# Kernel tuning notes

Measured on AMD Instinct MI355X. Metric: run time of the kernel, lower is better.

## Reference

```python
import jax, jax.numpy as jnp
import numpy as np

B, T, D = 4, 2048, 1024
H = 16
HD = D // H  # 64


def setup_inputs() -> dict:
    key = jax.random.key(0)
    ks = jax.random.split(key, 9)
    x = jax.random.normal(ks[0], (B, T, D), dtype=jnp.float32)
    s = 0.02
    Wq = jax.random.normal(ks[1], (D, D), dtype=jnp.float32) * s
    bq = jnp.zeros((D,), dtype=jnp.float32)
    Wk = jax.random.normal(ks[2], (D, D), dtype=jnp.float32) * s
    bk = jnp.zeros((D,), dtype=jnp.float32)
    Wv = jax.random.normal(ks[3], (D, D), dtype=jnp.float32) * s
    bv = jnp.zeros((D,), dtype=jnp.float32)
    Wo = jax.random.normal(ks[4], (D, D), dtype=jnp.float32) * s
    bo = jnp.zeros((D,), dtype=jnp.float32)
    return {"x": x, "Wq": Wq, "bq": bq, "Wk": Wk, "bk": bk,
            "Wv": Wv, "bv": bv, "Wo": Wo, "bo": bo}


def reference(x, Wq, bq, Wk, bk, Wv, bv, Wo, bo):
    Bn, Tn, Dn = x.shape
    # projections -> [B, H, T, HD]
    def split_heads(y):
        return y.reshape(Bn, Tn, H, HD).transpose(0, 2, 1, 3)
    Q = split_heads(x @ Wq + bq)
    K = split_heads(x @ Wk + bk)
    V = split_heads(x @ Wv + bv)
    scores = jnp.einsum('bhqd,bhkd->bhqk', Q, K) / jnp.sqrt(jnp.float32(HD))
    attn = jax.nn.softmax(scores, axis=-1)           # [B, H, T, T]
    attn_weights = attn.mean(axis=1)                 # [B, T, T] (head-averaged)
    out = jnp.einsum('bhqk,bhkd->bhqd', attn, V)     # [B, H, T, HD]
    out = out.transpose(0, 2, 1, 3).reshape(Bn, Tn, Dn)
    out = out @ Wo + bo                              # [B, T, D]
    # pooling weight: mean over query dim -> [B, 1, T] -> transpose -> [B, T, 1]
    pool_w = attn_weights.mean(axis=1, keepdims=True).transpose(0, 2, 1)
    pooled = (out * pool_w).sum(axis=1)              # [B, D]
    return pooled
```

## Files before the change

### kernel.cpp

```cpp
#include <hip/hip_runtime.h>
#include <hip/hip_bf16.h>
#include <stdint.h>

#define B_ 4
#define T_ 2048
#define D_ 1024
#define H_ 16
#define HD_ 64

#define QSCALE 0.1803368801111244f

typedef __bf16 bf16_t;
typedef __bf16 bf16x8 __attribute__((ext_vector_type(8)));
typedef __bf16 bf16x4 __attribute__((ext_vector_type(4)));
typedef float f32x4 __attribute__((ext_vector_type(4)));

__device__ __forceinline__ f32x4 mfma16(bf16x8 a, bf16x8 b, f32x4 c) {
  return __builtin_amdgcn_mfma_f32_16x16x32_bf16(a, b, c, 0, 0, 0);
}

__device__ __forceinline__ void gload_lds16(const bf16_t* g, bf16_t* l) {
  __builtin_amdgcn_global_load_lds(
      (const __attribute__((address_space(1))) unsigned int*)g,
      (__attribute__((address_space(3))) unsigned int*)l, 16, 0, 0);
}

__device__ __forceinline__ float exp2g(float x) {
  return __builtin_amdgcn_exp2f(x);
}

__global__ __launch_bounds__(256) void conv_x(const float* __restrict__ x,
                                              bf16_t* __restrict__ xb) {
  size_t i = ((size_t)blockIdx.x * 256 + threadIdx.x) * 8;
  float4 a = *(const float4*)(x + i);
  float4 b = *(const float4*)(x + i + 4);
  bf16x8 v;
  v[0] = (bf16_t)a.x; v[1] = (bf16_t)a.y; v[2] = (bf16_t)a.z; v[3] = (bf16_t)a.w;
  v[4] = (bf16_t)b.x; v[5] = (bf16_t)b.y; v[6] = (bf16_t)b.z; v[7] = (bf16_t)b.w;
  *(bf16x8*)(xb + i) = v;
}

__global__ __launch_bounds__(256) void conv_wt3(
    const float* __restrict__ Wq, const float* __restrict__ Wk,
    const float* __restrict__ Wv, bf16_t* __restrict__ WtAll) {
  __shared__ float Ls[64][65];
  const int tid = threadIdx.x;
  const int z = blockIdx.z;
  const float* W = (z == 0) ? Wq : (z == 1) ? Wk : Wv;
  bf16_t* Wt = WtAll + (size_t)z * 1024 * D_;
  const int k0 = blockIdx.y * 64, n0 = blockIdx.x * 64;
  const int rr = tid >> 4, cc = (tid & 15) * 4;
#pragma unroll
  for (int it = 0; it < 4; ++it) {
    int r = rr + it * 16;
    float4 v = *(const float4*)(W + (size_t)(k0 + r) * D_ + n0 + cc);
    Ls[r][cc] = v.x; Ls[r][cc + 1] = v.y; Ls[r][cc + 2] = v.z; Ls[r][cc + 3] = v.w;
  }
  __syncthreads();
#pragma unroll
  for (int it = 0; it < 4; ++it) {
    int nl = rr + it * 16;
    bf16x4 o;
    o[0] = (bf16_t)Ls[cc][nl];     o[1] = (bf16_t)Ls[cc + 1][nl];
    o[2] = (bf16_t)Ls[cc + 2][nl]; o[3] = (bf16_t)Ls[cc + 3][nl];
    *(bf16x4*)(Wt + (size_t)(n0 + nl) * D_ + k0 + cc) = o;
  }
}

__global__ __launch_bounds__(256) void gemm_qkv(
    const bf16_t* __restrict__ A, const bf16_t* __restrict__ Bt,
    const float* __restrict__ bq, const float* __restrict__ bk,
    const float* __restrict__ bv,
    bf16_t* __restrict__ Qo, bf16_t* __restrict__ Ko, bf16_t* __restrict__ Vo)
{
  __shared__ __align__(16) bf16_t As[128 * 64];
  __shared__ __align__(16) bf16_t Bs[128 * 64];
  const int tid = threadIdx.x, lane = tid & 63, wv = tid >> 6;
  const int wr = wv >> 1, wc = wv & 1;
  const int wg = blockIdx.x;
  const int xcd = wg & 7;
  const int local = wg >> 3;
  const int mb = xcd * 8 + (local & 7);
  const int nb = local >> 3;
  const int m0 = mb * 128, n0 = nb * 128;
  const int mode = nb >> 3;
  const int lr = lane & 15, lg = lane >> 4;
  const int srow = wv * 8 + (lane >> 3);
  const int scol = (lane & 7) * 8;

  f32x4 acc[4][4] = {};

  for (int k0 = 0; k0 < D_; k0 += 64) {
    __syncthreads();
#pragma unroll
    for (int i = 0; i < 4; ++i) {
      gload_lds16(A + (size_t)(m0 + i * 32 + srow) * D_ + k0 + scol,
                  &As[(i * 32 + wv * 8) * 64]);
      gload_lds16(Bt + (size_t)(n0 + i * 32 + srow) * D_ + k0 + scol,
                  &Bs[(i * 32 + wv * 8) * 64]);
    }
    __syncthreads();

#pragma unroll
    for (int ks = 0; ks < 2; ++ks) {
      bf16x8 af[4], bfr[4];
#pragma unroll
      for (int i = 0; i < 4; ++i)
        af[i] = *(const bf16x8*)&As[(wr * 64 + i * 16 + lr) * 64 + ks * 32 + lg * 8];
#pragma unroll
      for (int j = 0; j < 4; ++j)
        bfr[j] = *(const bf16x8*)&Bs[(wc * 64 + j * 16 + lr) * 64 + ks * 32 + lg * 8];
#pragma unroll
      for (int i = 0; i < 4; ++i)
#pragma unroll
        for (int j = 0; j < 4; ++j)
          acc[i][j] = mfma16(af[i], bfr[j], acc[i][j]);
    }
  }

  bf16_t* out = (mode == 0) ? Qo : (mode == 1) ? Ko : Vo;
  const float* bias = (mode == 0) ? bq : (mode == 1) ? bk : bv;
  const float scale = (mode == 0) ? QSCALE : 1.0f;
  const int nl0 = n0 - mode * 1024;
#pragma unroll
  for (int j = 0; j < 4; ++j) {
    int n = nl0 + wc * 64 + j * 16 + lr;
    float bval = bias[n];
    int h = n >> 6, d = n & 63;
#pragma unroll
    for (int i = 0; i < 4; ++i)
#pragma unroll
      for (int r = 0; r < 4; ++r) {
        int m = m0 + wr * 64 + i * 16 + lg * 4 + r;
        int b = m >> 11, t = m & (T_ - 1);
        float val = (acc[i][j][r] + bval) * scale;
        out[(((size_t)(b * H_ + h)) * T_ + t) * HD_ + d] = (bf16_t)val;
      }
  }
}

__global__ __launch_bounds__(256) void qkv_gemm_f32(
    const float* __restrict__ x, const float* __restrict__ W,
    const float* __restrict__ bias, bf16_t* __restrict__ out, float scale)
{
  __shared__ bf16_t As[128][40];
  __shared__ bf16_t Bs[128][40];
  const int tid = threadIdx.x, lane = tid & 63, wv = tid >> 6;
  const int wr = wv >> 1, wc = wv & 1;
  const int m0 = blockIdx.y * 128, n0 = blockIdx.x * 128;
  const int lr = lane & 15, lg = lane >> 4;
  f32x4 acc[4][4] = {};
  const int xr = tid >> 3, xc = tid & 7;
  const int wk = tid >> 5, wn = tid & 31;

  for (int k0 = 0; k0 < D_; k0 += 32) {
    __syncthreads();
#pragma unroll
    for (int it = 0; it < 4; ++it) {
      int r = xr + it * 32;
      float4 v = *(const float4*)(x + (size_t)(m0 + r) * D_ + k0 + xc * 4);
      bf16_t* dst = &As[r][xc * 4];
      dst[0] = (bf16_t)v.x; dst[1] = (bf16_t)v.y;
      dst[2] = (bf16_t)v.z; dst[3] = (bf16_t)v.w;
    }
#pragma unroll
    for (int it = 0; it < 4; ++it) {
      int k = wk + it * 8;
      float4 v = *(const float4*)(W + (size_t)(k0 + k) * D_ + n0 + wn * 4);
      Bs[wn * 4 + 0][k] = (bf16_t)v.x;
      Bs[wn * 4 + 1][k] = (bf16_t)v.y;
      Bs[wn * 4 + 2][k] = (bf16_t)v.z;
      Bs[wn * 4 + 3][k] = (bf16_t)v.w;
    }
    __syncthreads();
    bf16x8 af[4], bfr[4];
#pragma unroll
    for (int i = 0; i < 4; ++i) af[i]  = *(const bf16x8*)&As[wr * 64 + i * 16 + lr][lg * 8];
#pragma unroll
    for (int j = 0; j < 4; ++j) bfr[j] = *(const bf16x8*)&Bs[wc * 64 + j * 16 + lr][lg * 8];
#pragma unroll
    for (int i = 0; i < 4; ++i)
#pragma unroll
      for (int j = 0; j < 4; ++j)
        acc[i][j] = mfma16(af[i], bfr[j], acc[i][j]);
  }

#pragma unroll
  for (int j = 0; j < 4; ++j) {
    int n = n0 + wc * 64 + j * 16 + lr;
    float bval = bias[n];
    int h = n >> 6, d = n & 63;
#pragma unroll
    for (int i = 0; i < 4; ++i)
#pragma unroll
      for (int r = 0; r < 4; ++r) {
        int m = m0 + wr * 64 + i * 16 + lg * 4 + r;
        int b = m >> 11, t = m & (T_ - 1);
        float val = (acc[i][j][r] + bval) * scale;
        out[(((size_t)(b * H_ + h)) * T_ + t) * HD_ + d] = (bf16_t)val;
      }
  }
}

__global__ __launch_bounds__(256) void attn_rowsum(
    const bf16_t* __restrict__ Q, const bf16_t* __restrict__ K,
    float* __restrict__ Lsum)
{
  const int tid = threadIdx.x, lane = tid & 63, wv = tid >> 6;
  const int lr = lane & 15, lg = lane >> 4;
  const int wg = blockIdx.x;
  const int p_ = wg >> 3;
  const int bh = (wg & 7) * 8 + (p_ >> 4);
  const int rem = p_ & 15;
  const int qc = rem >> 1;
  const int th = rem & 1;
  const int q0w = qc * 256 + wv * 64;

  const bf16_t* Qb = Q + (size_t)bh * T_ * HD_;
  const bf16_t* Kb = K + (size_t)bh * T_ * HD_;

  bf16x8 qa[4][2];
#pragma unroll
  for (int qq = 0; qq < 4; ++qq)
#pragma unroll
    for (int ks = 0; ks < 2; ++ks)
      qa[qq][ks] = *(const bf16x8*)(Qb + (size_t)(q0w + qq * 16 + lr) * HD_ +
                                    ks * 32 + lg * 8);

  float acc[4][4] = {};

  const int tlo = th * (T_ / 2), thi = tlo + T_ / 2;
  for (int tb = tlo; tb < thi; tb += 64) {
#pragma unroll
    for (int ts = 0; ts < 2; ++ts) {
      const int tA = tb + ts * 32 + lr;
      const int tB = tA + 16;
      bf16x8 kA0 = *(const bf16x8*)(Kb + (size_t)tA * HD_ + lg * 8);
      bf16x8 kA1 = *(const bf16x8*)(Kb + (size_t)tA * HD_ + 32 + lg * 8);
      bf16x8 kB0 = *(const bf16x8*)(Kb + (size_t)tB * HD_ + lg * 8);
      bf16x8 kB1 = *(const bf16x8*)(Kb + (size_t)tB * HD_ + 32 + lg * 8);
#pragma unroll
      for (int qq = 0; qq < 4; ++qq) {
        f32x4 sA = {}, sB = {};
        __builtin_amdgcn_s_setprio(1);
        sA = mfma16(qa[qq][0], kA0, sA);
        sA = mfma16(qa[qq][1], kA1, sA);
        sB = mfma16(qa[qq][0], kB0, sB);
        sB = mfma16(qa[qq][1], kB1, sB);
        __builtin_amdgcn_s_setprio(0);
#pragma unroll
        for (int r = 0; r < 4; ++r)
          acc[qq][r] += exp2g(sA[r]) + exp2g(sB[r]);
      }
    }
  }

#pragma unroll
  for (int qq = 0; qq < 4; ++qq)
#pragma unroll
    for (int r = 0; r < 4; ++r) {
      float v = acc[qq][r];
      v += __shfl_xor(v, 1); v += __shfl_xor(v, 2);
      v += __shfl_xor(v, 4); v += __shfl_xor(v, 8);
      acc[qq][r] = v;
    }
  if (lr == 0) {
#pragma unroll
    for (int qq = 0; qq < 4; ++qq)
#pragma unroll
      for (int r = 0; r < 4; ++r)
        atomicAdd(&Lsum[(size_t)bh * T_ + q0w + qq * 16 + lg * 4 + r],
                  acc[qq][r]);
  }
}

__global__ __launch_bounds__(256) void inv_l(float* __restrict__ L) {
  size_t i = ((size_t)blockIdx.x * 256 + threadIdx.x) * 4;
  float4 v = *(float4*)(L + i);
  v.x = 1.f / v.x; v.y = 1.f / v.y; v.z = 1.f / v.z; v.w = 1.f / v.w;
  *(float4*)(L + i) = v;
}

__global__ __launch_bounds__(256) void attn_colsum(
    const bf16_t* __restrict__ Q, const bf16_t* __restrict__ K,
    const float* __restrict__ Linv, float* __restrict__ colsum)
{
  const int tid = threadIdx.x, lane = tid & 63, wv = tid >> 6;
  const int lr = lane & 15, lg = lane >> 4;
  const int wg = blockIdx.x;
  const int p_ = wg >> 3;
  const int bh = (wg & 7) * 8 + (p_ >> 4);
  const int rem = p_ & 15;
  const int tc = rem >> 2;
  const int qs = rem & 3;
  const int b = bh >> 4;
  const int t0w = tc * 512 + wv * 128;

  const bf16_t* Qb = Q + (size_t)bh * T_ * HD_;
  const bf16_t* Kb = K + (size_t)bh * T_ * HD_;
  const float* Lb = Linv + (size_t)bh * T_;

  bf16x8 kf[8][2];
#pragma unroll
  for (int tt = 0; tt < 8; ++tt)
#pragma unroll
    for (int ks = 0; ks < 2; ++ks)
      kf[tt][ks] = *(const bf16x8*)(Kb + (size_t)(t0w + tt * 16 + lr) * HD_ +
                                    ks * 32 + lg * 8);

  float acc[8][4] = {};

  const int qlo = qs * (T_ / 4), qhi = qlo + T_ / 4;
  for (int qb = qlo; qb < qhi; qb += 64) {
#pragma unroll
    for (int qp = 0; qp < 2; ++qp) {
      const int qA = qb + qp * 32 + lr;
      const int qB = qA + 16;
      bf16x8 qA0 = *(const bf16x8*)(Qb + (size_t)qA * HD_ + lg * 8);
      bf16x8 qA1 = *(const bf16x8*)(Qb + (size_t)qA * HD_ + 32 + lg * 8);
      bf16x8 qB0 = *(const bf16x8*)(Qb + (size_t)qB * HD_ + lg * 8);
      bf16x8 qB1 = *(const bf16x8*)(Qb + (size_t)qB * HD_ + 32 + lg * 8);
      const float lvA = Lb[qA];
      const float lvB = Lb[qB];
#pragma unroll
      for (int tt = 0; tt < 8; ++tt) {
        f32x4 sA = {}, sB = {};
        __builtin_amdgcn_s_setprio(1);
        sA = mfma16(kf[tt][0], qA0, sA);
        sA = mfma16(kf[tt][1], qA1, sA);
        sB = mfma16(kf[tt][0], qB0, sB);
        sB = mfma16(kf[tt][1], qB1, sB);
        __builtin_amdgcn_s_setprio(0);
#pragma unroll
        for (int r = 0; r < 4; ++r) {
          acc[tt][r] = fmaf(exp2g(sA[r]), lvA, acc[tt][r]);
          acc[tt][r] = fmaf(exp2g(sB[r]), lvB, acc[tt][r]);
        }
      }
    }
  }

#pragma unroll
  for (int tt = 0; tt < 8; ++tt)
#pragma unroll
    for (int r = 0; r < 4; ++r) {
      float v = acc[tt][r];
      v += __shfl_xor(v, 1); v += __shfl_xor(v, 2);
      v += __shfl_xor(v, 4); v += __shfl_xor(v, 8);
      acc[tt][r] = v;
    }
  if (lr == 0) {
#pragma unroll
    for (int tt = 0; tt < 8; ++tt)
#pragma unroll
      for (int r = 0; r < 4; ++r)
        atomicAdd(&colsum[b * T_ + t0w + tt * 16 + lg * 4 + r], acc[tt][r]);
  }
}

__global__ __launch_bounds__(256) void attn_w2(
    const bf16_t* __restrict__ Q, const bf16_t* __restrict__ K,
    const float* __restrict__ Linv, const float* __restrict__ CS,
    float* __restrict__ w2)
{
  const int tid = threadIdx.x, lane = tid & 63, wv = tid >> 6;
  const int lr = lane & 15, lg = lane >> 4;
  const int wg = blockIdx.x;
  const int p_ = wg >> 3;
  const int bh = (wg & 7) * 8 + (p_ >> 4);
  const int rem = p_ & 15;
  const int tc = rem >> 2;
  const int qs = rem & 3;
  const int b = bh >> 4;
  const int t0w = tc * 512 + wv * 128;

  const bf16_t* Qb = Q + (size_t)bh * T_ * HD_;
  const bf16_t* Kb = K + (size_t)bh * T_ * HD_;
  const float* Lb = Linv + (size_t)bh * T_;
  const float* Cb = CS + (size_t)b * T_;

  bf16x8 kf[8][2];
#pragma unroll
  for (int tt = 0; tt < 8; ++tt)
#pragma unroll
    for (int ks = 0; ks < 2; ++ks)
      kf[tt][ks] = *(const bf16x8*)(Kb + (size_t)(t0w + tt * 16 + lr) * HD_ +
                                    ks * 32 + lg * 8);

  float acc[8][4] = {};

  const int qlo = qs * (T_ / 4), qhi = qlo + T_ / 4;
  for (int qb = qlo; qb < qhi; qb += 64) {
#pragma unroll
    for (int qp = 0; qp < 2; ++qp) {
      const int qA = qb + qp * 32 + lr;
      const int qB = qA + 16;
      bf16x8 qA0 = *(const bf16x8*)(Qb + (size_t)qA * HD_ + lg * 8);
      bf16x8 qA1 = *(const bf16x8*)(Qb + (size_t)qA * HD_ + 32 + lg * 8);
      bf16x8 qB0 = *(const bf16x8*)(Qb + (size_t)qB * HD_ + lg * 8);
      bf16x8 qB1 = *(const bf16x8*)(Qb + (size_t)qB * HD_ + 32 + lg * 8);
      const float lvA = Cb[qA] * Lb[qA] * (1.f / 32768.f);
      const float lvB = Cb[qB] * Lb[qB] * (1.f / 32768.f);
#pragma unroll
      for (int tt = 0; tt < 8; ++tt) {
        f32x4 sA = {}, sB = {};
        __builtin_amdgcn_s_setprio(1);
        sA = mfma16(kf[tt][0], qA0, sA);
        sA = mfma16(kf[tt][1], qA1, sA);
        sB = mfma16(kf[tt][0], qB0, sB);
        sB = mfma16(kf[tt][1], qB1, sB);
        __builtin_amdgcn_s_setprio(0);
#pragma unroll
        for (int r = 0; r < 4; ++r) {
          acc[tt][r] = fmaf(exp2g(sA[r]), lvA, acc[tt][r]);
          acc[tt][r] = fmaf(exp2g(sB[r]), lvB, acc[tt][r]);
        }
      }
    }
  }

#pragma unroll
  for (int tt = 0; tt < 8; ++tt)
#pragma unroll
    for (int r = 0; r < 4; ++r) {
      float v = acc[tt][r];
      v += __shfl_xor(v, 1); v += __shfl_xor(v, 2);
      v += __shfl_xor(v, 4); v += __shfl_xor(v, 8);
      acc[tt][r] = v;
    }
  if (lr == 0) {
#pragma unroll
    for (int tt = 0; tt < 8; ++tt)
#pragma unroll
      for (int r = 0; r < 4; ++r)
        atomicAdd(&w2[(size_t)bh * T_ + t0w + tt * 16 + lg * 4 + r],
                  acc[tt][r]);
  }
}

__global__ __launch_bounds__(256) void pool_wv(
    const bf16_t* __restrict__ V, const float* __restrict__ W2,
    float* __restrict__ pre)
{
  __shared__ float sm[256];
  const int wg = blockIdx.x;
  const int bh = wg >> 3, sc = wg & 7;
  const int b = bh >> 4, h = bh & 15;
  const int tid = threadIdx.x, d = tid & 63, tg = tid >> 6;
  const bf16_t* Vb = V + (size_t)bh * T_ * HD_ + (size_t)sc * 256 * HD_;
  const float* wb = W2 + (size_t)bh * T_ + sc * 256;
  float acc = 0.f;
  for (int s = tg; s < 256; s += 4)
    acc += wb[s] * (float)Vb[(size_t)s * HD_ + d];
  sm[tid] = acc;
  __syncthreads();
  if (tid < 64) {
    float s = sm[tid] + sm[tid + 64] + sm[tid + 128] + sm[tid + 192];
    atomicAdd(&pre[b * D_ + h * 64 + tid], s);
  }
}

__global__ __launch_bounds__(256) void out_acc(
    const float* __restrict__ pre, const float* __restrict__ Wo,
    const float* __restrict__ bo, float* __restrict__ out)
{
  const int dc = blockIdx.x & 3, kb = blockIdx.x >> 2;
  const int d = dc * 256 + threadIdx.x;
  const int k0 = kb * 32;
  float acc0 = 0.f, acc1 = 0.f, acc2 = 0.f, acc3 = 0.f;
#pragma unroll
  for (int kk = 0; kk < 32; ++kk) {
    const int k = k0 + kk;
    const float w = Wo[(size_t)k * D_ + d];
    acc0 = fmaf(pre[k],            w, acc0);
    acc1 = fmaf(pre[D_ + k],       w, acc1);
    acc2 = fmaf(pre[2 * D_ + k],   w, acc2);
    acc3 = fmaf(pre[3 * D_ + k],   w, acc3);
  }
  if (kb == 0) {
    const float bd = bo[d];
    acc0 += bd; acc1 += bd; acc2 += bd; acc3 += bd;
  }
  atomicAdd(&out[d],           acc0);
  atomicAdd(&out[D_ + d],      acc1);
  atomicAdd(&out[2 * D_ + d],  acc2);
  atomicAdd(&out[3 * D_ + d],  acc3);
}

extern "C" void kernel_launch(void* const* d_in, const int* in_sizes, int n_in,
                              void* d_out, int out_size, void* d_ws, size_t ws_size,
                              hipStream_t stream)
{
  (void)in_sizes; (void)n_in; (void)out_size;
  const float* x  = (const float*)d_in[0];
  const float* Wq = (const float*)d_in[1];
  const float* bq = (const float*)d_in[2];
  const float* Wk = (const float*)d_in[3];
  const float* bk = (const float*)d_in[4];
  const float* Wv = (const float*)d_in[5];
  const float* bv = (const float*)d_in[6];
  const float* Wo = (const float*)d_in[7];
  const float* bo = (const float*)d_in[8];
  float* out = (float*)d_out;

  char* ws = (char*)d_ws;
  const size_t MB = 1ull << 20;
  const size_t KB = 1024;
  bf16_t* Qw = (bf16_t*)(ws);
  bf16_t* Kw = (bf16_t*)(ws + 16 * MB);
  bf16_t* Vw = (bf16_t*)(ws + 32 * MB);
  bf16_t* XB = (bf16_t*)(ws + 48 * MB);
  const size_t need_fast = 72 * MB;
  const bool fast = ws_size >= need_fast;

  size_t soff = fast ? 70 * MB : 64 * MB;
  float* LV  = (float*)(ws + soff);
  float* CS  = (float*)(ws + soff + 512 * KB);
  float* PRE = (float*)(ws + soff + 544 * KB);
  float* W2  = (float*)(ws + soff + 560 * KB);
  dim3 blk(256, 1, 1);

  if (fast) {
    bf16_t* WtAll = (bf16_t*)(ws + 64 * MB);
    conv_x<<<dim3((B_ * T_ * D_) / (256 * 8), 1, 1), blk, 0, stream>>>(x, XB);
    conv_wt3<<<dim3(16, 16, 3), blk, 0, stream>>>(Wq, Wk, Wv, WtAll);
    gemm_qkv<<<dim3(1536, 1, 1), blk, 0, stream>>>(XB, WtAll, bq, bk, bv,
                                                   Qw, Kw, Vw);
  } else {
    qkv_gemm_f32<<<dim3(8, 64, 1), blk, 0, stream>>>(x, Wq, bq, Qw, QSCALE);
    qkv_gemm_f32<<<dim3(8, 64, 1), blk, 0, stream>>>(x, Wk, bk, Kw, 1.0f);
    qkv_gemm_f32<<<dim3(8, 64, 1), blk, 0, stream>>>(x, Wv, bv, Vw, 1.0f);
  }

  hipMemsetAsync(LV, 0, 1072 * KB, stream);
  hipMemsetAsync(out, 0, (size_t)B_ * D_ * sizeof(float), stream);

  attn_rowsum<<<dim3(1024, 1, 1), blk, 0, stream>>>(Qw, Kw, LV);
  inv_l<<<dim3((B_ * H_ * T_) / (256 * 4), 1, 1), blk, 0, stream>>>(LV);
  attn_colsum<<<dim3(1024, 1, 1), blk, 0, stream>>>(Qw, Kw, LV, CS);
  attn_w2<<<dim3(1024, 1, 1), blk, 0, stream>>>(Qw, Kw, LV, CS, W2);
  pool_wv<<<dim3(512, 1, 1), blk, 0, stream>>>(Vw, W2, PRE);
  out_acc<<<dim3(128, 1, 1), blk, 0, stream>>>(PRE, Wo, bo, out);
}
```

Before: 301.1 us.

## Enlarge QKV GEMM tile to 256x128 with 512 threads and fold reciprocal into consumers

```diff
diff --git a/kernel.cpp b/kernel.cpp
--- a/kernel.cpp
+++ b/kernel.cpp
@@ -27,6 +27,10 @@
 
 __device__ __forceinline__ float exp2g(float x) {
   return __builtin_amdgcn_exp2f(x);
+}
+
+__device__ __forceinline__ float rcpg(float x) {
+  return __builtin_amdgcn_rcpf(x);
 }
 
 __global__ __launch_bounds__(256) void conv_x(const float* __restrict__ x,
@@ -67,38 +71,39 @@
   }
 }
 
-__global__ __launch_bounds__(256) void gemm_qkv(
+__global__ __launch_bounds__(512) void gemm_qkv(
     const bf16_t* __restrict__ A, const bf16_t* __restrict__ Bt,
     const float* __restrict__ bq, const float* __restrict__ bk,
     const float* __restrict__ bv,
     bf16_t* __restrict__ Qo, bf16_t* __restrict__ Ko, bf16_t* __restrict__ Vo)
 {
-  __shared__ __align__(16) bf16_t As[128 * 64];
+  __shared__ __align__(16) bf16_t As[256 * 64];
   __shared__ __align__(16) bf16_t Bs[128 * 64];
   const int tid = threadIdx.x, lane = tid & 63, wv = tid >> 6;
   const int wr = wv >> 1, wc = wv & 1;
   const int wg = blockIdx.x;
   const int xcd = wg & 7;
   const int local = wg >> 3;
-  const int mb = xcd * 8 + (local & 7);
-  const int nb = local >> 3;
-  const int m0 = mb * 128, n0 = nb * 128;
+  const int mb = xcd * 4 + (local & 3);
+  const int nb = local >> 2;
+  const int m0 = mb * 256, n0 = nb * 128;
   const int mode = nb >> 3;
   const int lr = lane & 15, lg = lane >> 4;
-  const int srow = wv * 8 + (lane >> 3);
-  const int scol = (lane & 7) * 8;
+  const int srow = tid >> 3;
+  const int scol = (tid & 7) * 8;
 
   f32x4 acc[4][4] = {};
 
   for (int k0 = 0; k0 < D_; k0 += 64) {
     __syncthreads();
 #pragma unroll
-    for (int i = 0; i < 4; ++i) {
-      gload_lds16(A + (size_t)(m0 + i * 32 + srow) * D_ + k0 + scol,
-                  &As[(i * 32 + wv * 8) * 64]);
-      gload_lds16(Bt + (size_t)(n0 + i * 32 + srow) * D_ + k0 + scol,
-                  &Bs[(i * 32 + wv * 8) * 64]);
-    }
+    for (int i = 0; i < 4; ++i)
+      gload_lds16(A + (size_t)(m0 + i * 64 + srow) * D_ + k0 + scol,
+                  &As[(i * 64 + (wv << 3)) * 64]);
+#pragma unroll
+    for (int i = 0; i < 2; ++i)
+      gload_lds16(Bt + (size_t)(n0 + i * 64 + srow) * D_ + k0 + scol,
+                  &Bs[(i * 64 + (wv << 3)) * 64]);
     __syncthreads();
 
 #pragma unroll
@@ -274,16 +279,9 @@
   }
 }
 
-__global__ __launch_bounds__(256) void inv_l(float* __restrict__ L) {
-  size_t i = ((size_t)blockIdx.x * 256 + threadIdx.x) * 4;
-  float4 v = *(float4*)(L + i);
-  v.x = 1.f / v.x; v.y = 1.f / v.y; v.z = 1.f / v.z; v.w = 1.f / v.w;
-  *(float4*)(L + i) = v;
-}
-
 __global__ __launch_bounds__(256) void attn_colsum(
     const bf16_t* __restrict__ Q, const bf16_t* __restrict__ K,
-    const float* __restrict__ Linv, float* __restrict__ colsum)
+    const float* __restrict__ Lsum, float* __restrict__ colsum)
 {
   const int tid = threadIdx.x, lane = tid & 63, wv = tid >> 6;
   const int lr = lane & 15, lg = lane >> 4;
@@ -298,7 +296,7 @@
 
   const bf16_t* Qb = Q + (size_t)bh * T_ * HD_;
   const bf16_t* Kb = K + (size_t)bh * T_ * HD_;
-  const float* Lb = Linv + (size_t)bh * T_;
+  const float* Lb = Lsum + (size_t)bh * T_;
 
   bf16x8 kf[8][2];
 #pragma unroll
@@ -320,8 +318,8 @@
       bf16x8 qA1 = *(const bf16x8*)(Qb + (size_t)qA * HD_ + 32 + lg * 8);
       bf16x8 qB0 = *(const bf16x8*)(Qb + (size_t)qB * HD_ + lg * 8);
       bf16x8 qB1 = *(const bf16x8*)(Qb + (size_t)qB * HD_ + 32 + lg * 8);
-      const float lvA = Lb[qA];
-      const float lvB = Lb[qB];
+      const float lvA = rcpg(Lb[qA]);
+      const float lvB = rcpg(Lb[qB]);
 #pragma unroll
       for (int tt = 0; tt < 8; ++tt) {
         f32x4 sA = {}, sB = {};
@@ -360,7 +358,7 @@
 
 __global__ __launch_bounds__(256) void attn_w2(
     const bf16_t* __restrict__ Q, const bf16_t* __restrict__ K,
-    const float* __restrict__ Linv, const float* __restrict__ CS,
+    const float* __restrict__ Lsum, const float* __restrict__ CS,
     float* __restrict__ w2)
 {
   const int tid = threadIdx.x, lane = tid & 63, wv = tid >> 6;
@@ -376,7 +374,7 @@
 
   const bf16_t* Qb = Q + (size_t)bh * T_ * HD_;
   const bf16_t* Kb = K + (size_t)bh * T_ * HD_;
-  const float* Lb = Linv + (size_t)bh * T_;
+  const float* Lb = Lsum + (size_t)bh * T_;
   const float* Cb = CS + (size_t)b * T_;
 
   bf16x8 kf[8][2];
@@ -399,8 +397,8 @@
       bf16x8 qA1 = *(const bf16x8*)(Qb + (size_t)qA * HD_ + 32 + lg * 8);
       bf16x8 qB0 = *(const bf16x8*)(Qb + (size_t)qB * HD_ + lg * 8);
       bf16x8 qB1 = *(const bf16x8*)(Qb + (size_t)qB * HD_ + 32 + lg * 8);
-      const float lvA = Cb[qA] * Lb[qA] * (1.f / 32768.f);
-      const float lvB = Cb[qB] * Lb[qB] * (1.f / 32768.f);
+      const float lvA = Cb[qA] * rcpg(Lb[qA]) * (1.f / 32768.f);
+      const float lvB = Cb[qB] * rcpg(Lb[qB]) * (1.f / 32768.f);
 #pragma unroll
       for (int tt = 0; tt < 8; ++tt) {
         f32x4 sA = {}, sB = {};
@@ -524,8 +522,8 @@
     bf16_t* WtAll = (bf16_t*)(ws + 64 * MB);
     conv_x<<<dim3((B_ * T_ * D_) / (256 * 8), 1, 1), blk, 0, stream>>>(x, XB);
     conv_wt3<<<dim3(16, 16, 3), blk, 0, stream>>>(Wq, Wk, Wv, WtAll);
-    gemm_qkv<<<dim3(1536, 1, 1), blk, 0, stream>>>(XB, WtAll, bq, bk, bv,
-                                                   Qw, Kw, Vw);
+    gemm_qkv<<<dim3(768, 1, 1), dim3(512, 1, 1), 0, stream>>>(
+        XB, WtAll, bq, bk, bv, Qw, Kw, Vw);
   } else {
     qkv_gemm_f32<<<dim3(8, 64, 1), blk, 0, stream>>>(x, Wq, bq, Qw, QSCALE);
     qkv_gemm_f32<<<dim3(8, 64, 1), blk, 0, stream>>>(x, Wk, bk, Kw, 1.0f);
@@ -536,7 +534,6 @@
   hipMemsetAsync(out, 0, (size_t)B_ * D_ * sizeof(float), stream);
 
   attn_rowsum<<<dim3(1024, 1, 1), blk, 0, stream>>>(Qw, Kw, LV);
-  inv_l<<<dim3((B_ * H_ * T_) / (256 * 4), 1, 1), blk, 0, stream>>>(LV);
   attn_colsum<<<dim3(1024, 1, 1), blk, 0, stream>>>(Qw, Kw, LV, CS);
   attn_w2<<<dim3(1024, 1, 1), blk, 0, stream>>>(Qw, Kw, LV, CS, W2);
   pool_wv<<<dim3(512, 1, 1), blk, 0, stream>>>(Vw, W2, PRE);
```

After: 296.9 us. No clear change (-1.4%).
